# Performance work log

Hardware: AMD Instinct MI355X
Metric: run time of the kernel (lower is better)

## Reference

```python
import jax, jax.numpy as jnp
import numpy as np

B, C = 4096, 1          # batch, num_clusters (C forced to 1 by the view in the original)
S = 2048                # sequence_length
AR = 8                  # ar_order
E = 8                   # exogenous_dim
RD = AR + E


def setup_inputs() -> dict:
    key = jax.random.key(0)
    k1, k2, k3 = jax.random.split(key, 3)
    y = jax.random.normal(k1, (B, C, AR + 1), dtype=jnp.float32)
    u = jax.random.normal(k2, (B, C, S + E), dtype=jnp.float32)
    W = jax.random.normal(k3, (C, RD), dtype=jnp.float32) * 0.05
    return {"y": y, "u": u, "W": W}


def reference(y, u, W):
    # Step i (i = 0..S-1, corresponding to t = AR+1+i) reads u[:, :, 1+i : 1+i+E].
    idx = 1 + jnp.arange(S)[:, None] + jnp.arange(E)[None, :]      # [S, E]
    u_win = jnp.transpose(u[:, :, idx], (2, 0, 1, 3))              # [S, B, C, E]

    w = W[0]  # [RD] — valid since num_clusters == 1 (required by original view)

    def step(window, u_t):
        # window: last AR+1 outputs, [B, C, AR+1]; u_t: [B, C, E]
        diffs = window[:, :, 1:] - window[:, :, :-1]               # [B, C, AR]
        reg = jnp.concatenate([diffs, u_t], axis=2)                # [B, C, RD]
        pred = jnp.einsum('bcr,r->bc', reg, w)                     # [B, C]
        new = window[:, :, -1] + pred                              # [B, C]
        new_window = jnp.concatenate([window[:, :, 1:], new[:, :, None]], axis=2)
        return new_window, new

    _, outs = jax.lax.scan(step, y, u_win)                         # outs: [S, B, C]
    out = jnp.concatenate([y, jnp.transpose(outs, (1, 2, 0))], axis=2)  # [B, C, S+AR+1]
    return out
```

## Files before the change

### kernel.cpp

```cpp
#include <hip/hip_runtime.h>

#define B_TOT 4096
#define S_LEN 2048
#define K_CH  64
#define L_CH  32
#define N_CK  (B_TOT * K_CH)
#define U_ROW (S_LEN + 8)
#define O_ROW (S_LEN + 9)

struct F4s { float a, b, c, d; };

template<int FINAL>
__global__ __launch_bounds__(256) void arix_chunk(
    const float* __restrict__ u, const float* __restrict__ W,
    float* __restrict__ ws, float* __restrict__ out)
{
    const int tid = blockIdx.x * 256 + threadIdx.x;
    const int k = tid & (K_CH - 1);
    const int b = tid >> 6;

    float wd[8], wu[8];
#pragma unroll
    for (int j = 0; j < 8; ++j) { wd[j] = W[j]; wu[j] = W[8 + j]; }

    const float* ub = u + (long)b * U_ROW + k * L_CH;

    float ua[L_CH + 8];
    {
        const float4* up = (const float4*)ub;
#pragma unroll
        for (int q = 0; q < (L_CH + 8) / 4; ++q) {
            float4 v = up[q];
            ua[4*q] = v.x; ua[4*q+1] = v.y; ua[4*q+2] = v.z; ua[4*q+3] = v.w;
        }
    }

    float dr[8], x;
    if (FINAL) {
#pragma unroll
        for (int i = 0; i < 8; ++i) dr[i] = ws[i * N_CK + tid];
        x = ws[8 * N_CK + tid];
    } else {
#pragma unroll
        for (int i = 0; i < 8; ++i) dr[i] = 0.f;
        x = 0.f;
    }

    float* ob = out + (long)b * O_ROW + 9 + k * L_CH;

#pragma unroll
    for (int s4 = 0; s4 < L_CH; s4 += 4) {
        float xo[4];
#pragma unroll
        for (int q = 0; q < 4; ++q) {
            const int s = s4 + q;
            float acc = wu[0] * ua[s + 1];
#pragma unroll
            for (int j = 1; j < 8; ++j) acc = fmaf(wu[j], ua[s + 1 + j], acc);
#pragma unroll
            for (int j = 0; j < 8; ++j) acc = fmaf(wd[j], dr[j], acc);
#pragma unroll
            for (int j = 0; j < 7; ++j) dr[j] = dr[j + 1];
            dr[7] = acc;
            x += acc;
            xo[q] = x;
        }
        if (FINAL) {
            F4s v = { xo[0], xo[1], xo[2], xo[3] };
            *(F4s*)(ob + s4) = v;
        }
    }

    if (!FINAL) {
#pragma unroll
        for (int i = 0; i < 8; ++i) ws[i * N_CK + tid] = dr[i];
        ws[8 * N_CK + tid] = x;
    }
}

__global__ __launch_bounds__(256) void arix_combine(
    const float* __restrict__ y, const float* __restrict__ W,
    float* __restrict__ ws, float* __restrict__ out)
{
    __shared__ float Msh[6 * 64];
    __shared__ float Csh[6 * 8];
    const int lt = threadIdx.x;

    if (lt < 8) {
        float wd[8];
#pragma unroll
        for (int i = 0; i < 8; ++i) wd[i] = W[i];
        float dr[8];
#pragma unroll
        for (int i = 0; i < 8; ++i) dr[i] = (i == lt) ? 1.f : 0.f;
        float xs = 0.f;
        for (int t = 0; t < L_CH; ++t) {
            float acc = wd[0] * dr[0];
#pragma unroll
            for (int i = 1; i < 8; ++i) acc = fmaf(wd[i], dr[i], acc);
#pragma unroll
            for (int i = 0; i < 7; ++i) dr[i] = dr[i + 1];
            dr[7] = acc; xs += acc;
        }
#pragma unroll
        for (int i = 0; i < 8; ++i) Msh[i * 8 + lt] = dr[i];
        Csh[lt] = xs;
    }
    __syncthreads();

    for (int l = 1; l < 6; ++l) {
        const float* Mp = Msh + (l - 1) * 64;
        const float* Cp = Csh + (l - 1) * 8;
        float mv = 0.f, cv = 0.f;
        if (lt < 64) {
            const int i = lt >> 3, j = lt & 7;
            float a = 0.f;
#pragma unroll
            for (int m = 0; m < 8; ++m) a = fmaf(Mp[i * 8 + m], Mp[m * 8 + j], a);
            mv = a;
        }
        if (lt < 8) {
            float a = Cp[lt];
#pragma unroll
            for (int i = 0; i < 8; ++i) a = fmaf(Cp[i], Mp[i * 8 + lt], a);
            cv = a;
        }
        __syncthreads();
        if (lt < 64) Msh[l * 64 + lt] = mv;
        if (lt < 8)  Csh[l * 8 + lt] = cv;
        __syncthreads();
    }

    const int tid = blockIdx.x * 256 + lt;
    const int k = lt & 63;
    const int b = tid >> 6;

    float P[8], Q;
#pragma unroll
    for (int i = 0; i < 8; ++i) P[i] = ws[i * N_CK + tid];
    Q = ws[8 * N_CK + tid];

    const float* yb = y + b * 9;
    float yv[9];
#pragma unroll
    for (int i = 0; i < 9; ++i) yv[i] = yb[i];
    float s0[8];
#pragma unroll
    for (int i = 0; i < 8; ++i) s0[i] = yv[i + 1] - yv[i];
    const float x0 = yv[8];

    if (k == 0) {
        float np[8];
#pragma unroll
        for (int i = 0; i < 8; ++i) {
            float a = P[i];
#pragma unroll
            for (int j = 0; j < 8; ++j) a = fmaf(Msh[i * 8 + j], s0[j], a);
            np[i] = a;
        }
        float qa = Q;
#pragma unroll
        for (int j = 0; j < 8; ++j) qa = fmaf(Csh[j], s0[j], qa);
#pragma unroll
        for (int i = 0; i < 8; ++i) P[i] = np[i];
        Q = qa;
    }

#pragma unroll
    for (int l = 0; l < 6; ++l) {
        const int delta = 1 << l;
        float Pl[8], Ql;
#pragma unroll
        for (int i = 0; i < 8; ++i) Pl[i] = __shfl_up(P[i], delta);
        Ql = __shfl_up(Q, delta);
        if (k >= delta) {
            const float* Mp = Msh + l * 64;
            const float* Cp = Csh + l * 8;
            float np[8];
#pragma unroll
            for (int i = 0; i < 8; ++i) {
                float a = P[i];
#pragma unroll
                for (int j = 0; j < 8; ++j) a = fmaf(Mp[i * 8 + j], Pl[j], a);
                np[i] = a;
            }
            float qa = Q + Ql;
#pragma unroll
            for (int j = 0; j < 8; ++j) qa = fmaf(Cp[j], Pl[j], qa);
#pragma unroll
            for (int i = 0; i < 8; ++i) P[i] = np[i];
            Q = qa;
        }
    }

    float Pin[8], Qin;
#pragma unroll
    for (int i = 0; i < 8; ++i) Pin[i] = __shfl_up(P[i], 1);
    Qin = __shfl_up(Q, 1);
    if (k == 0) {
#pragma unroll
        for (int i = 0; i < 8; ++i) Pin[i] = s0[i];
        Qin = 0.f;
    }

#pragma unroll
    for (int i = 0; i < 8; ++i) ws[i * N_CK + tid] = Pin[i];
    ws[8 * N_CK + tid] = x0 + Qin;

    if (k < 9) out[(long)b * O_ROW + k] = yv[k];
}

extern "C" void kernel_launch(void* const* d_in, const int* in_sizes, int n_in,
                              void* d_out, int out_size, void* d_ws, size_t ws_size,
                              hipStream_t stream) {
    const float* y = (const float*)d_in[0];
    const float* u = (const float*)d_in[1];
    const float* W = (const float*)d_in[2];
    float* out = (float*)d_out;
    float* ws = (float*)d_ws;

    arix_chunk<0><<<dim3(N_CK / 256), dim3(256), 0, stream>>>(u, W, ws, out);
    arix_combine<<<dim3(N_CK / 256), dim3(256), 0, stream>>>(y, W, ws, out);
    arix_chunk<1><<<dim3(N_CK / 256), dim3(256), 0, stream>>>(u, W, ws, out);
}
```

Baseline: 121.4 us.

## Fuse chunk scan, combine, and final pass into a single kernel

Merges the three kernels (local chunk recurrence, cross-chunk prefix combine, final recompute) into one kernel. Each thread keeps its u window and chunk state in registers, so the workspace round-trips through global memory and two kernel launches go away, and u is read once instead of twice. The cost is higher register pressure in one kernel (ua array, state and shuffle-scan values live together), which may lower occupancy.

```diff
diff --git a/kernel.cpp b/kernel.cpp
--- a/kernel.cpp
+++ b/kernel.cpp
@@ -4,27 +4,26 @@
 #define S_LEN 2048
 #define K_CH  64
 #define L_CH  32
-#define N_CK  (B_TOT * K_CH)
 #define U_ROW (S_LEN + 8)
 #define O_ROW (S_LEN + 9)
 
 struct F4s { float a, b, c, d; };
 
-template<int FINAL>
-__global__ __launch_bounds__(256) void arix_chunk(
-    const float* __restrict__ u, const float* __restrict__ W,
-    float* __restrict__ ws, float* __restrict__ out)
+__global__ __launch_bounds__(256) void arix_fused(
+    const float* __restrict__ y, const float* __restrict__ u,
+    const float* __restrict__ W, float* __restrict__ out)
 {
-    const int tid = blockIdx.x * 256 + threadIdx.x;
-    const int k = tid & (K_CH - 1);
-    const int b = tid >> 6;
+    __shared__ float Msh[6 * 64];
+    __shared__ float Csh[6 * 8];
+    const int lt = threadIdx.x;
+    const int k  = lt & 63;
+    const int b  = blockIdx.x * 4 + (lt >> 6);
 
     float wd[8], wu[8];
 #pragma unroll
     for (int j = 0; j < 8; ++j) { wd[j] = W[j]; wu[j] = W[8 + j]; }
 
     const float* ub = u + (long)b * U_ROW + k * L_CH;
-
     float ua[L_CH + 8];
     {
         const float4* up = (const float4*)ub;
@@ -34,62 +33,12 @@
             ua[4*q] = v.x; ua[4*q+1] = v.y; ua[4*q+2] = v.z; ua[4*q+3] = v.w;
         }
     }
-
-    float dr[8], x;
-    if (FINAL) {
+    const float* yb = y + b * 9;
+    float yv[9];
 #pragma unroll
-        for (int i = 0; i < 8; ++i) dr[i] = ws[i * N_CK + tid];
-        x = ws[8 * N_CK + tid];
-    } else {
-#pragma unroll
-        for (int i = 0; i < 8; ++i) dr[i] = 0.f;
-        x = 0.f;
-    }
-
-    float* ob = out + (long)b * O_ROW + 9 + k * L_CH;
-
-#pragma unroll
-    for (int s4 = 0; s4 < L_CH; s4 += 4) {
-        float xo[4];
-#pragma unroll
-        for (int q = 0; q < 4; ++q) {
-            const int s = s4 + q;
-            float acc = wu[0] * ua[s + 1];
-#pragma unroll
-            for (int j = 1; j < 8; ++j) acc = fmaf(wu[j], ua[s + 1 + j], acc);
-#pragma unroll
-            for (int j = 0; j < 8; ++j) acc = fmaf(wd[j], dr[j], acc);
-#pragma unroll
-            for (int j = 0; j < 7; ++j) dr[j] = dr[j + 1];
-            dr[7] = acc;
-            x += acc;
-            xo[q] = x;
-        }
-        if (FINAL) {
-            F4s v = { xo[0], xo[1], xo[2], xo[3] };
-            *(F4s*)(ob + s4) = v;
-        }
-    }
-
-    if (!FINAL) {
-#pragma unroll
-        for (int i = 0; i < 8; ++i) ws[i * N_CK + tid] = dr[i];
-        ws[8 * N_CK + tid] = x;
-    }
-}
-
-__global__ __launch_bounds__(256) void arix_combine(
-    const float* __restrict__ y, const float* __restrict__ W,
-    float* __restrict__ ws, float* __restrict__ out)
-{
-    __shared__ float Msh[6 * 64];
-    __shared__ float Csh[6 * 8];
-    const int lt = threadIdx.x;
+    for (int i = 0; i < 9; ++i) yv[i] = yb[i];
 
     if (lt < 8) {
-        float wd[8];
-#pragma unroll
-        for (int i = 0; i < 8; ++i) wd[i] = W[i];
         float dr[8];
 #pragma unroll
         for (int i = 0; i < 8; ++i) dr[i] = (i == lt) ? 1.f : 0.f;
@@ -107,7 +56,6 @@
         Csh[lt] = xs;
     }
     __syncthreads();
-
     for (int l = 1; l < 6; ++l) {
         const float* Mp = Msh + (l - 1) * 64;
         const float* Cp = Csh + (l - 1) * 8;
@@ -131,23 +79,30 @@
         __syncthreads();
     }
 
-    const int tid = blockIdx.x * 256 + lt;
-    const int k = lt & 63;
-    const int b = tid >> 6;
+    float dr[8], x = 0.f;
+#pragma unroll
+    for (int i = 0; i < 8; ++i) dr[i] = 0.f;
+#pragma unroll
+    for (int s = 0; s < L_CH; ++s) {
+        float acc = wu[0] * ua[s + 1];
+#pragma unroll
+        for (int j = 1; j < 8; ++j) acc = fmaf(wu[j], ua[s + 1 + j], acc);
+#pragma unroll
+        for (int j = 0; j < 8; ++j) acc = fmaf(wd[j], dr[j], acc);
+#pragma unroll
+        for (int j = 0; j < 7; ++j) dr[j] = dr[j + 1];
+        dr[7] = acc;
+        x += acc;
+    }
 
-    float P[8], Q;
-#pragma unroll
-    for (int i = 0; i < 8; ++i) P[i] = ws[i * N_CK + tid];
-    Q = ws[8 * N_CK + tid];
-
-    const float* yb = y + b * 9;
-    float yv[9];
-#pragma unroll
-    for (int i = 0; i < 9; ++i) yv[i] = yb[i];
     float s0[8];
 #pragma unroll
     for (int i = 0; i < 8; ++i) s0[i] = yv[i + 1] - yv[i];
     const float x0 = yv[8];
+
+    float P[8], Q = x;
+#pragma unroll
+    for (int i = 0; i < 8; ++i) P[i] = dr[i];
 
     if (k == 0) {
         float np[8];
@@ -204,8 +159,30 @@
     }
 
 #pragma unroll
-    for (int i = 0; i < 8; ++i) ws[i * N_CK + tid] = Pin[i];
-    ws[8 * N_CK + tid] = x0 + Qin;
+    for (int i = 0; i < 8; ++i) dr[i] = Pin[i];
+    x = x0 + Qin;
+
+    float* ob = out + (long)b * O_ROW + 9 + k * L_CH;
+#pragma unroll
+    for (int s4 = 0; s4 < L_CH; s4 += 4) {
+        float xo[4];
+#pragma unroll
+        for (int q = 0; q < 4; ++q) {
+            const int s = s4 + q;
+            float acc = wu[0] * ua[s + 1];
+#pragma unroll
+            for (int j = 1; j < 8; ++j) acc = fmaf(wu[j], ua[s + 1 + j], acc);
+#pragma unroll
+            for (int j = 0; j < 8; ++j) acc = fmaf(wd[j], dr[j], acc);
+#pragma unroll
+            for (int j = 0; j < 7; ++j) dr[j] = dr[j + 1];
+            dr[7] = acc;
+            x += acc;
+            xo[q] = x;
+        }
+        F4s v = { xo[0], xo[1], xo[2], xo[3] };
+        *(F4s*)(ob + s4) = v;
+    }
 
     if (k < 9) out[(long)b * O_ROW + k] = yv[k];
 }
@@ -217,9 +194,6 @@
     const float* u = (const float*)d_in[1];
     const float* W = (const float*)d_in[2];
     float* out = (float*)d_out;
-    float* ws = (float*)d_ws;
 
-    arix_chunk<0><<<dim3(N_CK / 256), dim3(256), 0, stream>>>(u, W, ws, out);
-    arix_combine<<<dim3(N_CK / 256), dim3(256), 0, stream>>>(y, W, ws, out);
-    arix_chunk<1><<<dim3(N_CK / 256), dim3(256), 0, stream>>>(u, W, ws, out);
+    arix_fused<<<dim3(B_TOT / 4), dim3(256), 0, stream>>>(y, u, W, out);
 }
```

Measured after the change: 99.28 us. -18.2%, faster.
